# Kernel tuning notes

Measured on AMD Instinct MI355X. Metric: run time of the kernel, lower is better.

The kernel has to match this reference:

```python
import jax, jax.numpy as jnp
import numpy as np

N_NODES = 100000
N_EDGES = 1600000
F_IN = 128
F_HID = 128
BN_EPS = 1e-5


def setup_inputs() -> dict:
    key = jax.random.key(0)
    ks = jax.random.split(key, 8)
    x = jax.random.normal(ks[0], (N_NODES, F_IN), dtype=jnp.float32)
    edge_row = jax.random.randint(ks[1], (N_EDGES,), 0, N_NODES, dtype=jnp.int32)
    edge_col = jax.random.randint(ks[2], (N_EDGES,), 0, N_NODES, dtype=jnp.int32)
    edge_weight = jax.random.uniform(ks[3], (N_EDGES,), dtype=jnp.float32)
    # Glorot-ish init for the two GCN layer weights
    W1 = jax.random.normal(ks[4], (F_IN, F_HID), dtype=jnp.float32) * (1.0 / np.sqrt(F_IN))
    b1 = jnp.zeros((F_HID,), dtype=jnp.float32)
    W2 = jax.random.normal(ks[5], (F_HID, F_HID), dtype=jnp.float32) * (1.0 / np.sqrt(F_HID))
    b2 = jnp.zeros((F_HID,), dtype=jnp.float32)
    gamma = jnp.ones((F_HID,), dtype=jnp.float32)
    beta = jnp.zeros((F_HID,), dtype=jnp.float32)
    return {"x": x, "edge_row": edge_row, "edge_col": edge_col,
            "edge_weight": edge_weight, "W1": W1, "b1": b1,
            "W2": W2, "b2": b2, "gamma": gamma, "beta": beta}


def _spmm(row, col, w, dense):
    # sparse [N,N] @ dense [N,F] via gather + segment_sum (COO)
    gathered = dense[col] * w[:, None]           # [E, F]
    return jax.ops.segment_sum(gathered, row, num_segments=N_NODES)


def _batchnorm(h, gamma, beta):
    # BatchNorm1d in training mode: batch statistics over node dim
    mean = jnp.mean(h, axis=0)
    var = jnp.var(h, axis=0)
    return gamma * (h - mean) * jax.lax.rsqrt(var + BN_EPS) + beta


def reference(x, edge_row, edge_col, edge_weight, W1, b1, W2, b2, gamma, beta):
    # Layer 1: GCN conv = adj @ (x @ W1) + b1
    h = _spmm(edge_row, edge_col, edge_weight, x @ W1) + b1
    # BN -> ReLU (dropout is identity in deterministic/eval reference)
    h = jax.nn.relu(_batchnorm(h, gamma, beta))
    # Layer 2: GCN conv
    out = _spmm(edge_row, edge_col, edge_weight, h @ W2) + b2
    return out
```

## Files before the change

kernel.cpp:

```cpp
#include <hip/hip_runtime.h>

#define F    128
#define FQ   32
#define FU   64
#define RPB  128
#define BSH  7
#define TILE 2048
#define SCAP 4096
#define LSTR 68

typedef __attribute__((ext_vector_type(8))) short short8;
typedef __attribute__((ext_vector_type(4))) float f32x4;

__device__ __forceinline__ unsigned int f2bf2(float a, float b) {
    unsigned int ua = __float_as_uint(a);
    unsigned int ub = __float_as_uint(b);
    ua = (ua + 0x7fffu + ((ua >> 16) & 1u)) >> 16;
    ub = (ub + 0x7fffu + ((ub >> 16) & 1u)) >> 16;
    return ua | (ub << 16);
}
__device__ __forceinline__ unsigned short f2bf1(float a) {
    unsigned int ua = __float_as_uint(a);
    return (unsigned short)((ua + 0x7fffu + ((ua >> 16) & 1u)) >> 16);
}

template <bool BN>
__global__ __launch_bounds__(256) void gemm_kernel(const void* __restrict__ Xv,
                                                   const float* __restrict__ W,
                                                   const float* __restrict__ ac,
                                                   unsigned int* __restrict__ Hb,
                                                   int nNodes) {
    __shared__ unsigned int XtU[64 * LSTR];
    __shared__ unsigned int WtU[128 * LSTR];

    const int tid = threadIdx.x;
    const int bn0 = blockIdx.x * 64;

    {
        int f = tid >> 1;
        int kh = (tid & 1) * 64;
        #pragma unroll
        for (int k8 = 0; k8 < 8; ++k8) {
            int k0 = kh + k8 * 8;
            float v[8];
            #pragma unroll
            for (int i = 0; i < 8; ++i) v[i] = W[(size_t)(k0 + i) * F + f];
            uint4 pk;
            pk.x = f2bf2(v[0], v[1]);
            pk.y = f2bf2(v[2], v[3]);
            pk.z = f2bf2(v[4], v[5]);
            pk.w = f2bf2(v[6], v[7]);
            *(uint4*)&WtU[f * LSTR + k0 / 2] = pk;
        }
    }
    {
        const float4* A4 = (const float4*)ac;
        const float4* C4 = (const float4*)(ac + F);
        #pragma unroll
        for (int it = 0; it < 8; ++it) {
            int i = tid + it * 256;
            int n = i >> 5;
            int kq = i & 31;
            int node = bn0 + n;
            uint2 pk = make_uint2(0u, 0u);
            if (BN) {
                uint2 raw = make_uint2(0u, 0u);
                if (node < nNodes) raw = ((const uint2*)Xv)[(size_t)node * 32 + kq];
                float4 v;
                v.x = __uint_as_float(raw.x << 16);
                v.y = __uint_as_float(raw.x & 0xffff0000u);
                v.z = __uint_as_float(raw.y << 16);
                v.w = __uint_as_float(raw.y & 0xffff0000u);
                float4 a = A4[kq], c = C4[kq];
                v.x = fmaxf(fmaf(a.x, v.x, c.x), 0.f);
                v.y = fmaxf(fmaf(a.y, v.y, c.y), 0.f);
                v.z = fmaxf(fmaf(a.z, v.z, c.z), 0.f);
                v.w = fmaxf(fmaf(a.w, v.w, c.w), 0.f);
                pk = make_uint2(f2bf2(v.x, v.y), f2bf2(v.z, v.w));
            } else {
                float4 v = make_float4(0.f, 0.f, 0.f, 0.f);
                if (node < nNodes) v = ((const float4*)Xv)[(size_t)node * FQ + kq];
                pk = make_uint2(f2bf2(v.x, v.y), f2bf2(v.z, v.w));
            }
            *(uint2*)&XtU[n * LSTR + kq * 2] = pk;
        }
    }
    __syncthreads();

    const int l = tid & 63;
    const int wv = tid >> 6;
    const int quad = l >> 4, lo = l & 15;
    const int fb = wv * 32;

    f32x4 acc[4][2];
    #pragma unroll
    for (int nt = 0; nt < 4; ++nt)
        #pragma unroll
        for (int ft = 0; ft < 2; ++ft) acc[nt][ft] = (f32x4){0.f, 0.f, 0.f, 0.f};

    #pragma unroll
    for (int kc = 0; kc < 4; ++kc) {
        int koff = kc * 16 + quad * 4;
        short8 a[4], b[2];
        #pragma unroll
        for (int nt = 0; nt < 4; ++nt)
            a[nt] = *(const short8*)&XtU[(nt * 16 + lo) * LSTR + koff];
        #pragma unroll
        for (int ft = 0; ft < 2; ++ft)
            b[ft] = *(const short8*)&WtU[(fb + ft * 16 + lo) * LSTR + koff];
        #pragma unroll
        for (int nt = 0; nt < 4; ++nt)
            #pragma unroll
            for (int ft = 0; ft < 2; ++ft)
                acc[nt][ft] = __builtin_amdgcn_mfma_f32_16x16x32_bf16(
                    a[nt], b[ft], acc[nt][ft], 0, 0, 0);
    }

    unsigned short* Hs = (unsigned short*)Hb;
    #pragma unroll
    for (int nt = 0; nt < 4; ++nt) {
        #pragma unroll
        for (int reg = 0; reg < 4; ++reg) {
            int node = bn0 + nt * 16 + quad * 4 + reg;
            if (node < nNodes) {
                #pragma unroll
                for (int ft = 0; ft < 2; ++ft)
                    Hs[(size_t)node * F + fb + ft * 16 + lo] = f2bf1(acc[nt][ft][reg]);
            }
        }
    }
}

__global__ __launch_bounds__(256) void histo_kernel(const int* __restrict__ row,
                                                    int* __restrict__ hist,
                                                    int NB, int E) {
    __shared__ int h[1024];
    int t = threadIdx.x;
    for (int i = t; i < NB; i += 256) h[i] = 0;
    __syncthreads();
    int base = blockIdx.x * TILE + t * 8;
    if (base + 7 < E) {
        int4 a = ((const int4*)row)[(base >> 2) + 0];
        int4 b = ((const int4*)row)[(base >> 2) + 1];
        atomicAdd(&h[a.x >> BSH], 1); atomicAdd(&h[a.y >> BSH], 1);
        atomicAdd(&h[a.z >> BSH], 1); atomicAdd(&h[a.w >> BSH], 1);
        atomicAdd(&h[b.x >> BSH], 1); atomicAdd(&h[b.y >> BSH], 1);
        atomicAdd(&h[b.z >> BSH], 1); atomicAdd(&h[b.w >> BSH], 1);
    } else {
        for (int j = 0; j < 8; ++j)
            if (base + j < E) atomicAdd(&h[row[base + j] >> BSH], 1);
    }
    __syncthreads();
    for (int i = t; i < NB; i += 256) hist[(size_t)blockIdx.x * NB + i] = h[i];
}

__global__ __launch_bounds__(256) void btot_kernel(const int* __restrict__ hist,
                                                   int* __restrict__ total,
                                                   int nT, int NB) {
    int b = blockIdx.x;
    int s = 0;
    for (int t = threadIdx.x; t < nT; t += 256) s += hist[(size_t)t * NB + b];
    __shared__ int red[256];
    red[threadIdx.x] = s;
    __syncthreads();
    for (int o = 128; o > 0; o >>= 1) {
        if (threadIdx.x < o) red[threadIdx.x] += red[threadIdx.x + o];
        __syncthreads();
    }
    if (threadIdx.x == 0) total[b] = red[0];
}

__global__ __launch_bounds__(1024) void bstart_kernel(const int* __restrict__ total,
                                                      int* __restrict__ start,
                                                      int NB, int E) {
    __shared__ int sh[1024];
    int t = threadIdx.x;
    int v = (t < NB) ? total[t] : 0;
    sh[t] = v;
    __syncthreads();
    #pragma unroll
    for (int o = 1; o < 1024; o <<= 1) {
        int add = (t >= o) ? sh[t - o] : 0;
        __syncthreads();
        sh[t] += add;
        __syncthreads();
    }
    if (t < NB) start[t] = sh[t] - v;
    if (t == 0) start[NB] = E;
}

__global__ __launch_bounds__(1024) void boff_kernel(const int* __restrict__ hist,
                                                    const int* __restrict__ start,
                                                    int* __restrict__ off,
                                                    int nT, int NB) {
    __shared__ int sh[1024];
    int b = blockIdx.x, t = threadIdx.x;
    int v = (t < nT) ? hist[(size_t)t * NB + b] : 0;
    sh[t] = v;
    __syncthreads();
    #pragma unroll
    for (int o = 1; o < 1024; o <<= 1) {
        int add = (t >= o) ? sh[t - o] : 0;
        __syncthreads();
        sh[t] += add;
        __syncthreads();
    }
    if (t < nT) off[(size_t)b * nT + t] = start[b] + sh[t] - v;
}

__global__ __launch_bounds__(256) void bplace_kernel(const int* __restrict__ row,
                                                     const int* __restrict__ col,
                                                     const float* __restrict__ w,
                                                     const int* __restrict__ off,
                                                     int2* __restrict__ tmp,
                                                     int nT, int NB, int E) {
    __shared__ int h[1024];
    int t = threadIdx.x, tile = blockIdx.x;
    for (int i = t; i < NB; i += 256) h[i] = 0;
    __syncthreads();
    int base = tile * TILE + t * 8;
    int r[8], c[8];
    float ww[8];
    int nv = 0;
    if (base + 7 < E) {
        int4 ra = ((const int4*)row)[(base >> 2) + 0];
        int4 rb = ((const int4*)row)[(base >> 2) + 1];
        int4 ca = ((const int4*)col)[(base >> 2) + 0];
        int4 cb = ((const int4*)col)[(base >> 2) + 1];
        float4 wa = ((const float4*)w)[(base >> 2) + 0];
        float4 wb = ((const float4*)w)[(base >> 2) + 1];
        r[0] = ra.x; r[1] = ra.y; r[2] = ra.z; r[3] = ra.w;
        r[4] = rb.x; r[5] = rb.y; r[6] = rb.z; r[7] = rb.w;
        c[0] = ca.x; c[1] = ca.y; c[2] = ca.z; c[3] = ca.w;
        c[4] = cb.x; c[5] = cb.y; c[6] = cb.z; c[7] = cb.w;
        ww[0] = wa.x; ww[1] = wa.y; ww[2] = wa.z; ww[3] = wa.w;
        ww[4] = wb.x; ww[5] = wb.y; ww[6] = wb.z; ww[7] = wb.w;
        nv = 8;
    } else {
        for (int j = 0; j < 8; ++j)
            if (base + j < E) { r[nv] = row[base + j]; c[nv] = col[base + j];
                                ww[nv] = w[base + j]; ++nv; }
    }
    #pragma unroll 8
    for (int j = 0; j < 8; ++j) {
        if (j >= nv) break;
        int b = r[j] >> BSH;
        int rank = atomicAdd(&h[b], 1);
        int pos = off[(size_t)b * nT + tile] + rank;
        tmp[pos] = make_int2(((r[j] & (RPB - 1)) << 25) | c[j], __float_as_int(ww[j]));
    }
}

__global__ __launch_bounds__(256) void bsort_kernel(const int2* __restrict__ tmp,
                                                    const int* __restrict__ start,
                                                    int2* __restrict__ pairs,
                                                    int* __restrict__ rowptr,
                                                    int N, int NB, int E) {
    __shared__ int cntB[RPB];
    __shared__ int cntS[RPB];
    __shared__ int sc[RPB];
    __shared__ int2 outP[SCAP];
    int b = blockIdx.x, t = threadIdx.x;
    int s0 = start[b], s1 = start[b + 1];
    int len = s1 - s0;
    if (len > SCAP) len = SCAP;

    if (t < RPB) cntB[t] = 0;
    __syncthreads();

    int2 p[16];
    int np = 0;
    #pragma unroll
    for (int k = 0; k < 16; ++k) {
        int i = t + k * 256;
        if (i < len) { p[k] = tmp[s0 + i]; ++np; }
    }
    #pragma unroll
    for (int k = 0; k < 16; ++k) {
        if (k >= np) break;
        atomicAdd(&cntB[((unsigned)p[k].x) >> 25], 1);
    }
    __syncthreads();
    int val = (t < RPB) ? cntB[t] : 0;
    if (t < RPB) sc[t] = val;
    __syncthreads();
    #pragma unroll
    for (int o = 1; o < RPB; o <<= 1) {
        int add = (t < RPB && t >= o) ? sc[t - o] : 0;
        __syncthreads();
        if (t < RPB) sc[t] += add;
        __syncthreads();
    }
    if (t < RPB) { int ex = sc[t] - val; cntB[t] = ex; cntS[t] = ex; }
    __syncthreads();
    #pragma unroll
    for (int k = 0; k < 16; ++k) {
        if (k >= np) break;
        int rl = ((unsigned)p[k].x) >> 25;
        int lr = atomicAdd(&cntB[rl], 1);
        outP[lr] = make_int2(p[k].x & 0x1ffffff, p[k].y);
    }
    __syncthreads();
    for (int i = t; i < len; i += 256) pairs[s0 + i] = outP[i];
    int r0 = b * RPB;
    if (t < RPB && r0 + t < N) rowptr[r0 + t] = s0 + cntS[t];
    if (b == NB - 1 && t == 0) rowptr[N] = E;
}

template <bool BF16OUT>
__global__ __launch_bounds__(256) void spmm_csr_kernel(const int* __restrict__ rowptr,
                                                       const int2* __restrict__ pairs,
                                                       const unsigned int* __restrict__ Hb,
                                                       const float* __restrict__ bias,
                                                       void* __restrict__ outv, int N) {
    int r = blockIdx.x * 4 + (threadIdx.x >> 6);
    if (r >= N) return;
    const int l = threadIdx.x & 63;
    const int g = l >> 4, q = l & 15;
    const uint4* H4 = (const uint4*)Hb;

    float acc[8];
    #pragma unroll
    for (int j = 0; j < 8; ++j) acc[j] = 0.f;

    int i = rowptr[r], end = rowptr[r + 1];

    for (; i + 16 <= end; i += 16) {
        int2 p[4];
        uint4 gv[4];
        #pragma unroll
        for (int k = 0; k < 4; ++k) p[k] = pairs[i + 4 * k + g];
        #pragma unroll
        for (int k = 0; k < 4; ++k) gv[k] = H4[(size_t)p[k].x * 16 + q];
        #pragma unroll
        for (int k = 0; k < 4; ++k) {
            float wt = __int_as_float(p[k].y);
            unsigned int uu[4] = {gv[k].x, gv[k].y, gv[k].z, gv[k].w};
            #pragma unroll
            for (int j = 0; j < 4; ++j) {
                acc[2 * j]     = fmaf(wt, __uint_as_float(uu[j] << 16), acc[2 * j]);
                acc[2 * j + 1] = fmaf(wt, __uint_as_float(uu[j] & 0xffff0000u), acc[2 * j + 1]);
            }
        }
    }
    for (; i + 4 <= end; i += 4) {
        int2 p = pairs[i + g];
        uint4 gv = H4[(size_t)p.x * 16 + q];
        float wt = __int_as_float(p.y);
        unsigned int uu[4] = {gv.x, gv.y, gv.z, gv.w};
        #pragma unroll
        for (int j = 0; j < 4; ++j) {
            acc[2 * j]     = fmaf(wt, __uint_as_float(uu[j] << 16), acc[2 * j]);
            acc[2 * j + 1] = fmaf(wt, __uint_as_float(uu[j] & 0xffff0000u), acc[2 * j + 1]);
        }
    }
    if (i < end) {
        int e = i + g;
        int2 p = (e < end) ? pairs[e] : make_int2(0, 0);
        uint4 gv = H4[(size_t)p.x * 16 + q];
        float wt = __int_as_float(p.y);
        unsigned int uu[4] = {gv.x, gv.y, gv.z, gv.w};
        #pragma unroll
        for (int j = 0; j < 4; ++j) {
            acc[2 * j]     = fmaf(wt, __uint_as_float(uu[j] << 16), acc[2 * j]);
            acc[2 * j + 1] = fmaf(wt, __uint_as_float(uu[j] & 0xffff0000u), acc[2 * j + 1]);
        }
    }

    #pragma unroll
    for (int j = 0; j < 8; ++j) {
        acc[j] += __shfl_xor(acc[j], 16, 64);
        acc[j] += __shfl_xor(acc[j], 32, 64);
    }

    if (g == 0) {
        if (bias) {
            float4 b0 = ((const float4*)bias)[q * 2];
            float4 b1 = ((const float4*)bias)[q * 2 + 1];
            acc[0] += b0.x; acc[1] += b0.y; acc[2] += b0.z; acc[3] += b0.w;
            acc[4] += b1.x; acc[5] += b1.y; acc[6] += b1.z; acc[7] += b1.w;
        }
        if (BF16OUT) {
            uint4 pk;
            pk.x = f2bf2(acc[0], acc[1]);
            pk.y = f2bf2(acc[2], acc[3]);
            pk.z = f2bf2(acc[4], acc[5]);
            pk.w = f2bf2(acc[6], acc[7]);
            ((uint4*)outv)[(size_t)r * 16 + q] = pk;
        } else {
            float4* o = (float4*)outv;
            o[(size_t)r * 32 + q * 2]     = make_float4(acc[0], acc[1], acc[2], acc[3]);
            o[(size_t)r * 32 + q * 2 + 1] = make_float4(acc[4], acc[5], acc[6], acc[7]);
        }
    }
}

__global__ __launch_bounds__(256) void bnstats_kernel(const unsigned int* __restrict__ Hu,
                                                      float* __restrict__ sums,
                                                      int nNodes) {
    int u = threadIdx.x & 63;
    int g = threadIdx.x >> 6;
    int stride = gridDim.x * 4;
    float s0 = 0.f, s1 = 0.f, q0 = 0.f, q1 = 0.f;
    for (int n = blockIdx.x * 4 + g; n < nNodes; n += stride) {
        unsigned int v = Hu[(size_t)n * FU + u];
        float a = __uint_as_float(v << 16);
        float b = __uint_as_float(v & 0xffff0000u);
        s0 += a; s1 += b;
        q0 = fmaf(a, a, q0); q1 = fmaf(b, b, q1);
    }
    __shared__ float4 red[256];
    red[threadIdx.x] = make_float4(s0, s1, q0, q1);
    __syncthreads();
    if (g == 0) {
        float4 r0 = red[u], r1 = red[64 + u], r2 = red[128 + u], r3 = red[192 + u];
        atomicAdd(&sums[2 * u],       r0.x + r1.x + r2.x + r3.x);
        atomicAdd(&sums[2 * u + 1],   r0.y + r1.y + r2.y + r3.y);
        atomicAdd(&sums[128 + 2 * u],     r0.z + r1.z + r2.z + r3.z);
        atomicAdd(&sums[128 + 2 * u + 1], r0.w + r1.w + r2.w + r3.w);
    }
}

__global__ void bnfinal_kernel(const float* __restrict__ sums,
                               const float* __restrict__ gamma,
                               const float* __restrict__ beta,
                               float* __restrict__ ac, float invN) {
    int f = threadIdx.x;
    float mean = sums[f] * invN;
    float var = sums[128 + f] * invN - mean * mean;
    float a = gamma[f] * rsqrtf(var + 1e-5f);
    ac[f] = a;
    ac[128 + f] = beta[f] - mean * a;
}

extern "C" void kernel_launch(void* const* d_in, const int* in_sizes, int n_in,
                              void* d_out, int out_size, void* d_ws, size_t ws_size,
                              hipStream_t stream) {
    const float* x    = (const float*)d_in[0];
    const int*   erow = (const int*)d_in[1];
    const int*   ecol = (const int*)d_in[2];
    const float* ew   = (const float*)d_in[3];
    const float* W1   = (const float*)d_in[4];
    const float* W2   = (const float*)d_in[6];
    const float* b2   = (const float*)d_in[7];
    const float* gmm  = (const float*)d_in[8];
    const float* beta = (const float*)d_in[9];
    float* out = (float*)d_out;

    const int N = in_sizes[0] / F;
    const int E = in_sizes[1];

    const int NB = (N + RPB - 1) / RPB;
    const int nT = (E + TILE - 1) / TILE;

    unsigned int* buf1   = (unsigned int*)d_ws;
    unsigned int* Hb     = buf1 + (size_t)N * FU;
    float*        stats  = (float*)(Hb + (size_t)N * FU);
    float*        ac     = stats + 256;
    int*          rowptr = (int*)(ac + 256);
    int*          start  = rowptr + N + 2;
    int*          total  = start + 1028;
    int*          hist   = total + 1024;
    int*          off    = hist + (size_t)nT * NB;
    int2*         tmp    = (int2*)(off + (size_t)NB * nT);
    int2*         pairs  = tmp + E;

    const int gemmGrid = (N + 63) / 64;
    const int spmmGrid = (N + 3) / 4;

    hipMemsetAsync(stats, 0, 256 * sizeof(float), stream);

    histo_kernel<<<nT, 256, 0, stream>>>(erow, hist, NB, E);
    btot_kernel<<<NB, 256, 0, stream>>>(hist, total, nT, NB);
    bstart_kernel<<<1, 1024, 0, stream>>>(total, start, NB, E);
    boff_kernel<<<NB, 1024, 0, stream>>>(hist, start, off, nT, NB);
    bplace_kernel<<<nT, 256, 0, stream>>>(erow, ecol, ew, off, tmp, nT, NB, E);
    bsort_kernel<<<NB, 256, 0, stream>>>(tmp, start, pairs, rowptr, N, NB, E);

    gemm_kernel<false><<<gemmGrid, 256, 0, stream>>>(x, W1, nullptr, Hb, N);
    spmm_csr_kernel<true><<<spmmGrid, 256, 0, stream>>>(rowptr, pairs, Hb,
                                                        nullptr, buf1, N);
    bnstats_kernel<<<400, 256, 0, stream>>>(buf1, stats, N);
    bnfinal_kernel<<<1, 128, 0, stream>>>(stats, gmm, beta, ac, 1.0f / (float)N);
    gemm_kernel<true><<<gemmGrid, 256, 0, stream>>>(buf1, W2, ac, Hb, N);
    spmm_csr_kernel<false><<<spmmGrid, 256, 0, stream>>>(rowptr, pairs, Hb,
                                                         b2, out, N);
}
```

Baseline: 398.8 us.

## Store hidden features in sliced layout and split SpMM by feature slice

Hidden feature matrices are now stored in eight column slices of 16 bf16 features each, node-major within a slice. The SpMM launches eight blocks per row group, one per slice, so each block's gathers stay inside a smaller slice footprint, aiming for better cache locality on random column access. The BN finalize kernel is folded into the second GEMM's prologue, and nontemporal loads and stores are used for edge pairs and outputs. In exchange, every row's edge list is re-read once per slice, and each gather now moves only 32 bytes per node.

```diff
diff --git a/kernel.cpp b/kernel.cpp
--- a/kernel.cpp
+++ b/kernel.cpp
@@ -11,6 +11,7 @@
 
 typedef __attribute__((ext_vector_type(8))) short short8;
 typedef __attribute__((ext_vector_type(4))) float f32x4;
+typedef __attribute__((ext_vector_type(4))) unsigned int u32x4;
 
 __device__ __forceinline__ unsigned int f2bf2(float a, float b) {
     unsigned int ua = __float_as_uint(a);
@@ -27,7 +28,10 @@
 template <bool BN>
 __global__ __launch_bounds__(256) void gemm_kernel(const void* __restrict__ Xv,
                                                    const float* __restrict__ W,
-                                                   const float* __restrict__ ac,
+                                                   const float* __restrict__ stats,
+                                                   const float* __restrict__ gamma,
+                                                   const float* __restrict__ beta,
+                                                   float invN,
                                                    unsigned int* __restrict__ Hb,
                                                    int nNodes) {
     __shared__ unsigned int XtU[64 * LSTR];
@@ -54,35 +58,45 @@
         }
     }
     {
-        const float4* A4 = (const float4*)ac;
-        const float4* C4 = (const float4*)(ac + F);
+        const int kqc = tid & 31;
+        float4 a4, c4;
+        if (BN) {
+            float4 s  = ((const float4*)stats)[kqc];
+            float4 sq = ((const float4*)(stats + 128))[kqc];
+            float4 g4 = ((const float4*)gamma)[kqc];
+            float4 b4 = ((const float4*)beta)[kqc];
+            float m;
+            m = s.x * invN; a4.x = g4.x * rsqrtf(sq.x * invN - m * m + 1e-5f); c4.x = b4.x - m * a4.x;
+            m = s.y * invN; a4.y = g4.y * rsqrtf(sq.y * invN - m * m + 1e-5f); c4.y = b4.y - m * a4.y;
+            m = s.z * invN; a4.z = g4.z * rsqrtf(sq.z * invN - m * m + 1e-5f); c4.z = b4.z - m * a4.z;
+            m = s.w * invN; a4.w = g4.w * rsqrtf(sq.w * invN - m * m + 1e-5f); c4.w = b4.w - m * a4.w;
+        }
         #pragma unroll
         for (int it = 0; it < 8; ++it) {
             int i = tid + it * 256;
             int n = i >> 5;
-            int kq = i & 31;
             int node = bn0 + n;
             uint2 pk = make_uint2(0u, 0u);
             if (BN) {
                 uint2 raw = make_uint2(0u, 0u);
-                if (node < nNodes) raw = ((const uint2*)Xv)[(size_t)node * 32 + kq];
+                if (node < nNodes)
+                    raw = ((const uint2*)Xv)[((size_t)(kqc >> 2) * nNodes + node) * 4 + (kqc & 3)];
                 float4 v;
                 v.x = __uint_as_float(raw.x << 16);
                 v.y = __uint_as_float(raw.x & 0xffff0000u);
                 v.z = __uint_as_float(raw.y << 16);
                 v.w = __uint_as_float(raw.y & 0xffff0000u);
-                float4 a = A4[kq], c = C4[kq];
-                v.x = fmaxf(fmaf(a.x, v.x, c.x), 0.f);
-                v.y = fmaxf(fmaf(a.y, v.y, c.y), 0.f);
-                v.z = fmaxf(fmaf(a.z, v.z, c.z), 0.f);
-                v.w = fmaxf(fmaf(a.w, v.w, c.w), 0.f);
+                v.x = fmaxf(fmaf(a4.x, v.x, c4.x), 0.f);
+                v.y = fmaxf(fmaf(a4.y, v.y, c4.y), 0.f);
+                v.z = fmaxf(fmaf(a4.z, v.z, c4.z), 0.f);
+                v.w = fmaxf(fmaf(a4.w, v.w, c4.w), 0.f);
                 pk = make_uint2(f2bf2(v.x, v.y), f2bf2(v.z, v.w));
             } else {
                 float4 v = make_float4(0.f, 0.f, 0.f, 0.f);
-                if (node < nNodes) v = ((const float4*)Xv)[(size_t)node * FQ + kq];
+                if (node < nNodes) v = ((const float4*)Xv)[(size_t)node * FQ + kqc];
                 pk = make_uint2(f2bf2(v.x, v.y), f2bf2(v.z, v.w));
             }
-            *(uint2*)&XtU[n * LSTR + kq * 2] = pk;
+            *(uint2*)&XtU[n * LSTR + kqc * 2] = pk;
         }
     }
     __syncthreads();
@@ -125,7 +139,8 @@
             if (node < nNodes) {
                 #pragma unroll
                 for (int ft = 0; ft < 2; ++ft)
-                    Hs[(size_t)node * F + fb + ft * 16 + lo] = f2bf1(acc[nt][ft][reg]);
+                    Hs[((size_t)(wv * 2 + ft) * nNodes + node) * 16 + lo] =
+                        f2bf1(acc[nt][ft][reg]);
             }
         }
     }
@@ -308,45 +323,37 @@
 }
 
 template <bool BF16OUT>
-__global__ __launch_bounds__(256) void spmm_csr_kernel(const int* __restrict__ rowptr,
-                                                       const int2* __restrict__ pairs,
-                                                       const unsigned int* __restrict__ Hb,
-                                                       const float* __restrict__ bias,
-                                                       void* __restrict__ outv, int N) {
-    int r = blockIdx.x * 4 + (threadIdx.x >> 6);
-    if (r >= N) return;
-    const int l = threadIdx.x & 63;
-    const int g = l >> 4, q = l & 15;
-    const uint4* H4 = (const uint4*)Hb;
+__global__ __launch_bounds__(256) void spmm_sl_kernel(const int* __restrict__ rowptr,
+                                                      const int2* __restrict__ pairs,
+                                                      const unsigned int* __restrict__ Hsl,
+                                                      const float* __restrict__ bias,
+                                                      void* __restrict__ outv, int N) {
+    const int slice = blockIdx.x & 7;
+    const int rb    = blockIdx.x >> 3;
+    const int l     = threadIdx.x & 63;
+    const int wv    = threadIdx.x >> 6;
+    const int rsub  = l >> 5;
+    const int slot  = (l >> 1) & 15;
+    const int half  = l & 1;
+    const int r     = rb * 8 + wv * 2 + rsub;
+
+    const uint4* H4 = (const uint4*)Hsl + (size_t)slice * N * 2;
 
     float acc[8];
     #pragma unroll
     for (int j = 0; j < 8; ++j) acc[j] = 0.f;
 
-    int i = rowptr[r], end = rowptr[r + 1];
-
-    for (; i + 16 <= end; i += 16) {
-        int2 p[4];
-        uint4 gv[4];
-        #pragma unroll
-        for (int k = 0; k < 4; ++k) p[k] = pairs[i + 4 * k + g];
-        #pragma unroll
-        for (int k = 0; k < 4; ++k) gv[k] = H4[(size_t)p[k].x * 16 + q];
-        #pragma unroll
-        for (int k = 0; k < 4; ++k) {
-            float wt = __int_as_float(p[k].y);
-            unsigned int uu[4] = {gv[k].x, gv[k].y, gv[k].z, gv[k].w};
-            #pragma unroll
-            for (int j = 0; j < 4; ++j) {
-                acc[2 * j]     = fmaf(wt, __uint_as_float(uu[j] << 16), acc[2 * j]);
-                acc[2 * j + 1] = fmaf(wt, __uint_as_float(uu[j] & 0xffff0000u), acc[2 * j + 1]);
-            }
-        }
-    }
-    for (; i + 4 <= end; i += 4) {
-        int2 p = pairs[i + g];
-        uint4 gv = H4[(size_t)p.x * 16 + q];
-        float wt = __int_as_float(p.y);
+    int i0 = 0, end = 0;
+    if (r < N) { i0 = rowptr[r]; end = rowptr[r + 1]; }
+
+    for (int i = i0; i < end; i += 16) {
+        int e = i + slot;
+        long long pv = 0;
+        if (e < end)
+            pv = __builtin_nontemporal_load((const long long*)(pairs + e));
+        unsigned int col = (unsigned int)((unsigned long long)pv & 0xffffffffull);
+        float wt = __uint_as_float((unsigned int)(((unsigned long long)pv) >> 32));
+        uint4 gv = H4[(size_t)col * 2 + half];
         unsigned int uu[4] = {gv.x, gv.y, gv.z, gv.w};
         #pragma unroll
         for (int j = 0; j < 4; ++j) {
@@ -354,43 +361,37 @@
             acc[2 * j + 1] = fmaf(wt, __uint_as_float(uu[j] & 0xffff0000u), acc[2 * j + 1]);
         }
     }
-    if (i < end) {
-        int e = i + g;
-        int2 p = (e < end) ? pairs[e] : make_int2(0, 0);
-        uint4 gv = H4[(size_t)p.x * 16 + q];
-        float wt = __int_as_float(p.y);
-        unsigned int uu[4] = {gv.x, gv.y, gv.z, gv.w};
-        #pragma unroll
-        for (int j = 0; j < 4; ++j) {
-            acc[2 * j]     = fmaf(wt, __uint_as_float(uu[j] << 16), acc[2 * j]);
-            acc[2 * j + 1] = fmaf(wt, __uint_as_float(uu[j] & 0xffff0000u), acc[2 * j + 1]);
-        }
-    }
 
     #pragma unroll
     for (int j = 0; j < 8; ++j) {
+        acc[j] += __shfl_xor(acc[j], 2, 64);
+        acc[j] += __shfl_xor(acc[j], 4, 64);
+        acc[j] += __shfl_xor(acc[j], 8, 64);
         acc[j] += __shfl_xor(acc[j], 16, 64);
-        acc[j] += __shfl_xor(acc[j], 32, 64);
-    }
-
-    if (g == 0) {
+    }
+
+    if (slot == 0 && r < N) {
+        const int fb = slice * 16 + half * 8;
         if (bias) {
-            float4 b0 = ((const float4*)bias)[q * 2];
-            float4 b1 = ((const float4*)bias)[q * 2 + 1];
+            float4 b0 = ((const float4*)bias)[fb >> 2];
+            float4 b1 = ((const float4*)bias)[(fb >> 2) + 1];
             acc[0] += b0.x; acc[1] += b0.y; acc[2] += b0.z; acc[3] += b0.w;
             acc[4] += b1.x; acc[5] += b1.y; acc[6] += b1.z; acc[7] += b1.w;
         }
         if (BF16OUT) {
-            uint4 pk;
+            u32x4 pk;
             pk.x = f2bf2(acc[0], acc[1]);
             pk.y = f2bf2(acc[2], acc[3]);
             pk.z = f2bf2(acc[4], acc[5]);
             pk.w = f2bf2(acc[6], acc[7]);
-            ((uint4*)outv)[(size_t)r * 16 + q] = pk;
+            u32x4* O = (u32x4*)outv;
+            __builtin_nontemporal_store(pk, &O[((size_t)slice * N + r) * 2 + half]);
         } else {
-            float4* o = (float4*)outv;
-            o[(size_t)r * 32 + q * 2]     = make_float4(acc[0], acc[1], acc[2], acc[3]);
-            o[(size_t)r * 32 + q * 2 + 1] = make_float4(acc[4], acc[5], acc[6], acc[7]);
+            f32x4 v0 = (f32x4){acc[0], acc[1], acc[2], acc[3]};
+            f32x4 v1 = (f32x4){acc[4], acc[5], acc[6], acc[7]};
+            f32x4* O = (f32x4*)outv;
+            __builtin_nontemporal_store(v0, &O[(size_t)r * 32 + (fb >> 2)]);
+            __builtin_nontemporal_store(v1, &O[(size_t)r * 32 + (fb >> 2) + 1]);
         }
     }
 }
@@ -400,10 +401,11 @@
                                                       int nNodes) {
     int u = threadIdx.x & 63;
     int g = threadIdx.x >> 6;
+    const unsigned int* base = Hu + (size_t)(u >> 3) * nNodes * 8 + (u & 7);
     int stride = gridDim.x * 4;
     float s0 = 0.f, s1 = 0.f, q0 = 0.f, q1 = 0.f;
     for (int n = blockIdx.x * 4 + g; n < nNodes; n += stride) {
-        unsigned int v = Hu[(size_t)n * FU + u];
+        unsigned int v = base[(size_t)n * 8];
         float a = __uint_as_float(v << 16);
         float b = __uint_as_float(v & 0xffff0000u);
         s0 += a; s1 += b;
@@ -414,23 +416,12 @@
     __syncthreads();
     if (g == 0) {
         float4 r0 = red[u], r1 = red[64 + u], r2 = red[128 + u], r3 = red[192 + u];
-        atomicAdd(&sums[2 * u],       r0.x + r1.x + r2.x + r3.x);
-        atomicAdd(&sums[2 * u + 1],   r0.y + r1.y + r2.y + r3.y);
-        atomicAdd(&sums[128 + 2 * u],     r0.z + r1.z + r2.z + r3.z);
-        atomicAdd(&sums[128 + 2 * u + 1], r0.w + r1.w + r2.w + r3.w);
-    }
-}
-
-__global__ void bnfinal_kernel(const float* __restrict__ sums,
-                               const float* __restrict__ gamma,
-                               const float* __restrict__ beta,
-                               float* __restrict__ ac, float invN) {
-    int f = threadIdx.x;
-    float mean = sums[f] * invN;
-    float var = sums[128 + f] * invN - mean * mean;
-    float a = gamma[f] * rsqrtf(var + 1e-5f);
-    ac[f] = a;
-    ac[128 + f] = beta[f] - mean * a;
+        int f0 = (u >> 3) * 16 + (u & 7) * 2;
+        atomicAdd(&sums[f0],           r0.x + r1.x + r2.x + r3.x);
+        atomicAdd(&sums[f0 + 1],       r0.y + r1.y + r2.y + r3.y);
+        atomicAdd(&sums[128 + f0],     r0.z + r1.z + r2.z + r3.z);
+        atomicAdd(&sums[128 + f0 + 1], r0.w + r1.w + r2.w + r3.w);
+    }
 }
 
 extern "C" void kernel_launch(void* const* d_in, const int* in_sizes, int n_in,
@@ -456,8 +447,7 @@
     unsigned int* buf1   = (unsigned int*)d_ws;
     unsigned int* Hb     = buf1 + (size_t)N * FU;
     float*        stats  = (float*)(Hb + (size_t)N * FU);
-    float*        ac     = stats + 256;
-    int*          rowptr = (int*)(ac + 256);
+    int*          rowptr = (int*)(stats + 256);
     int*          start  = rowptr + N + 2;
     int*          total  = start + 1028;
     int*          hist   = total + 1024;
@@ -466,7 +456,7 @@
     int2*         pairs  = tmp + E;
 
     const int gemmGrid = (N + 63) / 64;
-    const int spmmGrid = (N + 3) / 4;
+    const int spmmGrid = ((N + 7) / 8) * 8;
 
     hipMemsetAsync(stats, 0, 256 * sizeof(float), stream);
 
@@ -477,12 +467,13 @@
     bplace_kernel<<<nT, 256, 0, stream>>>(erow, ecol, ew, off, tmp, nT, NB, E);
     bsort_kernel<<<NB, 256, 0, stream>>>(tmp, start, pairs, rowptr, N, NB, E);
 
-    gemm_kernel<false><<<gemmGrid, 256, 0, stream>>>(x, W1, nullptr, Hb, N);
-    spmm_csr_kernel<true><<<spmmGrid, 256, 0, stream>>>(rowptr, pairs, Hb,
-                                                        nullptr, buf1, N);
+    gemm_kernel<false><<<gemmGrid, 256, 0, stream>>>(x, W1, nullptr, nullptr,
+                                                     nullptr, 0.f, Hb, N);
+    spmm_sl_kernel<true><<<spmmGrid, 256, 0, stream>>>(rowptr, pairs, Hb,
+                                                       nullptr, buf1, N);
     bnstats_kernel<<<400, 256, 0, stream>>>(buf1, stats, N);
-    bnfinal_kernel<<<1, 128, 0, stream>>>(stats, gmm, beta, ac, 1.0f / (float)N);
-    gemm_kernel<true><<<gemmGrid, 256, 0, stream>>>(buf1, W2, ac, Hb, N);
-    spmm_csr_kernel<false><<<spmmGrid, 256, 0, stream>>>(rowptr, pairs, Hb,
-                                                         b2, out, N);
-}
+    gemm_kernel<true><<<gemmGrid, 256, 0, stream>>>(buf1, W2, stats, gmm, beta,
+                                                    1.0f / (float)N, Hb, N);
+    spmm_sl_kernel<false><<<spmmGrid, 256, 0, stream>>>(rowptr, pairs, Hb,
+                                                        b2, out, N);
+}
```

Measured after the change: 641.1 us. 1.61x slower.
